# Performance work log

Hardware: AMD Instinct MI355X
Metric: run time of the kernel (lower is better)

The kernel has to match this reference:

```python
import jax, jax.numpy as jnp
import numpy as np

B, T, E, H, S = 64, 128, 256, 512, 1024


def setup_inputs() -> dict:
    key = jax.random.key(0)
    ks = jax.random.split(key, 14)
    p = lambda k, shape, s=0.05: jax.random.normal(k, shape, dtype=jnp.float32) * s
    return {
        "embedded_inputs": jax.random.normal(ks[0], (B, T, E), dtype=jnp.float32),
        "h0": jax.random.normal(ks[1], (B, H), dtype=jnp.float32),
        "c0": jax.random.normal(ks[2], (B, H), dtype=jnp.float32),
        "context": jax.random.normal(ks[3], (B, S, H), dtype=jnp.float32),
        "W_ih": p(ks[4], (E, 4 * H)),
        "b_ih": p(ks[5], (4 * H,)),
        "W_hh": p(ks[6], (H, 4 * H)),
        "b_hh": p(ks[7], (4 * H,)),
        "W_out": p(ks[8], (2 * H, H)),
        "b_out": p(ks[9], (H,)),
        "W_ax": p(ks[10], (H + E, H)),
        "b_ax": p(ks[11], (H,)),
        "W_pg": p(ks[12], (4 * H, 1)),
        "b_pg": p(ks[13], (1,)),
    }


def reference(embedded_inputs, h0, c0, context, W_ih, b_ih, W_hh, b_hh,
              W_out, b_out, W_ax, b_ax, W_pg, b_pg):
    # mask positions where the encoder output is all-zero padding
    ctx_mask = jnp.mean(context, axis=-1) == 0  # [B,S]

    def step(carry, x):  # x: [B,E]
        h, c = carry
        gates = x @ W_ih + b_ih + h @ W_hh + b_hh          # [B,4H]
        i, f, g, o = jnp.split(gates, 4, axis=-1)
        c_t = jax.nn.sigmoid(f) * c + jax.nn.sigmoid(i) * jnp.tanh(g)
        h_t = jax.nn.sigmoid(o) * jnp.tanh(c_t)            # [B,H]
        # dot attention
        scores = jnp.einsum('bsh,bh->bs', context, h_t)    # [B,S]
        scores = jnp.where(ctx_mask, -jnp.inf, scores)
        attn_dist = jax.nn.softmax(scores, axis=1)         # [B,S]
        attn_ctx = jnp.einsum('bsh,bs->bh', context, attn_dist)  # [B,H]
        xa = jnp.concatenate([attn_ctx, x], axis=-1) @ W_ax + b_ax   # [B,H]
        out = jnp.concatenate([attn_ctx, h_t], axis=-1) @ W_out + b_out  # [B,H]
        p_gen = jax.nn.sigmoid(
            jnp.concatenate([attn_ctx, h_t, c_t, xa], axis=-1) @ W_pg + b_pg)  # [B,1]
        return (h_t, c_t), (out, attn_dist, p_gen)

    xs = jnp.swapaxes(embedded_inputs, 0, 1)  # [T,B,E]
    (h, c), (outputs, attn_dists, p_gens) = jax.lax.scan(step, (h0, c0), xs)
    return outputs, h, c, attn_dists, p_gens
```

## Files before the change

kernel.cpp:

```cpp
#include <hip/hip_runtime.h>

#define T_ 128
#define B_ 64
#define E_ 256
#define H_ 512
#define S_ 1024
#define G_ 2048
#define NCH 6
#define NBLK 512
#define ABLK 128
#define BLK 256
#define NGRP 16
#define BH (B_*H_)
#define PSTR 520
#define PARTBUF (B_*NCH*PSTR)

#define U_ARR   256
#define U_TOTAL (U_ARR + NBLK*16)

#define F_V1   8704
#define F_VX   (F_V1 + 512)
#define F_S0   (F_VX + 256)
#define F_H3   (F_S0 + 64)
#define F_C3   (F_H3 + 3*BH)
#define F_SC2  (F_C3 + 3*BH)
#define F_PART (F_SC2 + 2*B_*S_)
#define F_CTX16 (F_PART + 2*PARTBUF)
#define WS_MIN_BYTES ((size_t)F_CTX16*4)
#define WS_BF16_BYTES ((size_t)F_CTX16*4 + (size_t)B_*S_*H_*2)

#define O_OUT 0
#define O_H   ((size_t)T_*B_*H_)
#define O_C   (O_H + BH)
#define O_AD  (O_C + BH)
#define O_PG  (O_AD + (size_t)T_*B_*S_)

#define S_ACT   0
#define S_PART  3088
#define S_GATE  4112
#define SB_RED  0
#define SB_ML   2080
#define SB_BIAS 2088
#define C_ACTX  5136
#define C_H2    5648
#define C_PRT   6160
#define C_TMP   6416
#define C_V1    6424
#define POOLSZ  7200

#define NEG_INF (-__builtin_inff())

__device__ __forceinline__ float sigm(float x){ return 1.f/(1.f+__expf(-x)); }
__device__ __forceinline__ float tanh_(float x){ return 1.f - 2.f/(1.f+__expf(2.f*x)); }
__device__ __forceinline__ float wred(float v){
#pragma unroll
  for (int m = 1; m < 64; m <<= 1) v += __shfl_xor(v, m, 64);
  return v;
}
__device__ __forceinline__ float ald(const float* p){
  return __hip_atomic_load(p, __ATOMIC_RELAXED, __HIP_MEMORY_SCOPE_AGENT);
}
__device__ __forceinline__ void ast(float* p, float v){
  __hip_atomic_store(p, v, __ATOMIC_RELAXED, __HIP_MEMORY_SCOPE_AGENT);
}
__device__ __forceinline__ void ast64(unsigned long long* p, unsigned long long v){
  __hip_atomic_store(p, v, __ATOMIC_RELAXED, __HIP_MEMORY_SCOPE_AGENT);
}
__device__ __forceinline__ unsigned short b16rne(float f){
  unsigned u = __float_as_uint(f);
  unsigned r = u + 0x7fffu + ((u >> 16) & 1u);
  return (unsigned short)(r >> 16);
}
__device__ __forceinline__ void unp(unsigned w, float& lo, float& hi){
  lo = __uint_as_float(w << 16);
  hi = __uint_as_float(w & 0xffff0000u);
}

__device__ __forceinline__ void gbar(unsigned* W, unsigned ep){
  __syncthreads();
  const int tid = threadIdx.x, bid = blockIdx.x;
  if (tid == 0) {
    asm volatile("s_waitcnt vmcnt(0)" ::: "memory");
    __hip_atomic_store(&W[U_ARR + bid*16], ep, __ATOMIC_RELAXED, __HIP_MEMORY_SCOPE_AGENT);
  }
  if (bid == 0) {
    const int i0 = tid*2, i1 = i0+1;
    while (__hip_atomic_load(&W[U_ARR + i0*16], __ATOMIC_RELAXED, __HIP_MEMORY_SCOPE_AGENT) < ep)
      __builtin_amdgcn_s_sleep(2);
    while (__hip_atomic_load(&W[U_ARR + i1*16], __ATOMIC_RELAXED, __HIP_MEMORY_SCOPE_AGENT) < ep)
      __builtin_amdgcn_s_sleep(2);
    __syncthreads();
    if (tid < NGRP)
      __hip_atomic_store(&W[tid*16], ep, __ATOMIC_RELAXED, __HIP_MEMORY_SCOPE_AGENT);
  }
  if (tid == 0) {
    while (__hip_atomic_load(&W[(bid>>5)*16], __ATOMIC_RELAXED, __HIP_MEMORY_SCOPE_AGENT) < ep)
      __builtin_amdgcn_s_sleep(4);
  }
  __syncthreads();
}

__device__ void do_A(int t, int bid, int tid,
                     const float* __restrict__ emb, const float* __restrict__ Wih,
                     const float* __restrict__ bih, const float* __restrict__ Whh,
                     const float* __restrict__ bhh, float* __restrict__ F,
                     float* __restrict__ pool)
{
  const int bg = bid >> 3, ug = bid & 7;
  {
    const int r = tid >> 6, i = tid & 63;
    const float* xr = emb + ((size_t)(bg*4 + r)*T_ + t)*E_ + i*4;
    *(float4*)(pool + S_ACT + r*772 + i*4) = *(const float4*)xr;
    const float* hsrc = F + F_H3 + ((t+2)%3)*BH + (size_t)(bg*4 + r)*H_ + i*8;
    float4 h0v, h1v;
    h0v.x=ald(hsrc+0); h0v.y=ald(hsrc+1); h0v.z=ald(hsrc+2); h0v.w=ald(hsrc+3);
    h1v.x=ald(hsrc+4); h1v.y=ald(hsrc+5); h1v.z=ald(hsrc+6); h1v.w=ald(hsrc+7);
    *(float4*)(pool + S_ACT + r*772 + 256 + i*8)     = h0v;
    *(float4*)(pool + S_ACT + r*772 + 256 + i*8 + 4) = h1v;
  }
  __syncthreads();
  const int ks = tid >> 7, bl = (tid >> 5) & 3, cq = tid & 31;
  const int cgi1 = cq, cgi2 = cq + 32;
  const int col1 = ((cgi1 >> 4) << 9) + ug*64 + ((cgi1 & 15) << 2);
  const int col2 = ((cgi2 >> 4) << 9) + ug*64 + ((cgi2 & 15) << 2);
  float4 A1, A2;
  if (ks == 0) {
    const float4 x1 = *(const float4*)(bih + col1), y1 = *(const float4*)(bhh + col1);
    const float4 x2 = *(const float4*)(bih + col2), y2 = *(const float4*)(bhh + col2);
    A1.x=x1.x+y1.x; A1.y=x1.y+y1.y; A1.z=x1.z+y1.z; A1.w=x1.w+y1.w;
    A2.x=x2.x+y2.x; A2.y=x2.y+y2.y; A2.z=x2.z+y2.z; A2.w=x2.w+y2.w;
  } else { A1.x=A1.y=A1.z=A1.w=0.f; A2.x=A2.y=A2.z=A2.w=0.f; }
  const float* ap = pool + S_ACT + bl*772;
  if (ks == 0) {
    const float* w1 = Wih + col1; const float* w2 = Wih + col2;
#pragma unroll 8
    for (int k = 0; k < 256; ++k) {
      float a = ap[k];
      float4 v1 = *(const float4*)(w1 + (size_t)k*G_);
      float4 v2 = *(const float4*)(w2 + (size_t)k*G_);
      A1.x=fmaf(a,v1.x,A1.x); A1.y=fmaf(a,v1.y,A1.y); A1.z=fmaf(a,v1.z,A1.z); A1.w=fmaf(a,v1.w,A1.w);
      A2.x=fmaf(a,v2.x,A2.x); A2.y=fmaf(a,v2.y,A2.y); A2.z=fmaf(a,v2.z,A2.z); A2.w=fmaf(a,v2.w,A2.w);
    }
    const float* u1 = Whh + col1; const float* u2 = Whh + col2;
    const float* ap2 = ap + 256;
#pragma unroll 8
    for (int k = 0; k < 128; ++k) {
      float a = ap2[k];
      float4 v1 = *(const float4*)(u1 + (size_t)k*G_);
      float4 v2 = *(const float4*)(u2 + (size_t)k*G_);
      A1.x=fmaf(a,v1.x,A1.x); A1.y=fmaf(a,v1.y,A1.y); A1.z=fmaf(a,v1.z,A1.z); A1.w=fmaf(a,v1.w,A1.w);
      A2.x=fmaf(a,v2.x,A2.x); A2.y=fmaf(a,v2.y,A2.y); A2.z=fmaf(a,v2.z,A2.z); A2.w=fmaf(a,v2.w,A2.w);
    }
  } else {
    const float* u1 = Whh + (size_t)128*G_ + col1; const float* u2 = Whh + (size_t)128*G_ + col2;
    const float* ap2 = ap + 384;
#pragma unroll 8
    for (int k = 0; k < 384; ++k) {
      float a = ap2[k];
      float4 v1 = *(const float4*)(u1 + (size_t)k*G_);
      float4 v2 = *(const float4*)(u2 + (size_t)k*G_);
      A1.x=fmaf(a,v1.x,A1.x); A1.y=fmaf(a,v1.y,A1.y); A1.z=fmaf(a,v1.z,A1.z); A1.w=fmaf(a,v1.w,A1.w);
      A2.x=fmaf(a,v2.x,A2.x); A2.y=fmaf(a,v2.y,A2.y); A2.z=fmaf(a,v2.z,A2.z); A2.w=fmaf(a,v2.w,A2.w);
    }
  }
  if (ks == 1) {
    *(float4*)(pool + S_PART + ((bl*64 + cgi1) << 2)) = A1;
    *(float4*)(pool + S_PART + ((bl*64 + cgi2) << 2)) = A2;
  }
  __syncthreads();
  if (ks == 0) {
    const float4 P1 = *(const float4*)(pool + S_PART + ((bl*64 + cgi1) << 2));
    const float4 P2 = *(const float4*)(pool + S_PART + ((bl*64 + cgi2) << 2));
    A1.x+=P1.x; A1.y+=P1.y; A1.z+=P1.z; A1.w+=P1.w;
    A2.x+=P2.x; A2.y+=P2.y; A2.z+=P2.z; A2.w+=P2.w;
    *(float4*)(pool + S_GATE + bl*256 + (cgi1 << 2)) = A1;
    *(float4*)(pool + S_GATE + bl*256 + (cgi2 << 2)) = A2;
  }
  __syncthreads();
  {
    const int bl2 = tid >> 6, ul = tid & 63;
    const int b2 = bg*4 + bl2, uu = ug*64 + ul;
    float gi = pool[S_GATE + bl2*256 + ul];
    float gf = pool[S_GATE + bl2*256 + 64 + ul];
    float gg = pool[S_GATE + bl2*256 + 128 + ul];
    float go = pool[S_GATE + bl2*256 + 192 + ul];
    float cp = ald(F + F_C3 + ((t+2)%3)*BH + (size_t)b2*H_ + uu);
    float cn = sigm(gf)*cp + sigm(gi)*tanh_(gg);
    float hn = sigm(go)*tanh_(cn);
    ast(F + F_H3 + (t%3)*BH + (size_t)b2*H_ + uu, hn);
    ast(F + F_C3 + (t%3)*BH + (size_t)b2*H_ + uu, cn);
  }
}

template<bool BF16>
__device__ void do_B(int t, int bid, int tid, const float* __restrict__ ctx,
                     float* __restrict__ F, float* __restrict__ pool)
{
  const int idx = bid - ABLK;
  const int b = idx / NCH, ch = idx - b*NCH;
  const int sb = (ch*S_)/NCH, se = ((ch+1)*S_)/NCH;
  const int w = tid >> 6, lane = tid & 63;
  const float* hb = F + F_H3 + (t%3)*BH + (size_t)b*H_ + lane*8;
  float h0_=ald(hb+0), h1_=ald(hb+1), h2_=ald(hb+2), h3_=ald(hb+3),
        h4_=ald(hb+4), h5_=ald(hb+5), h6_=ald(hb+6), h7_=ald(hb+7);
  float* scw = F + F_SC2 + (size_t)(t&1)*(B_*S_) + (size_t)b*S_;
  const float* s_bias = pool + SB_BIAS;

  if (BF16) {
    const uint4* c16v = (const uint4*)(F + F_CTX16) + (size_t)b*S_*64 + lane;
    float l = 0.f;
    float a0=0,a1=0,a2=0,a3=0,a4=0,a5=0,a6=0,a7=0;
    for (int s0 = sb + w*16; s0 < se; s0 += 64) {
      uint4 q[16];
#pragma unroll
      for (int i = 0; i < 16; ++i) {
        int s = s0 + i;
        int ss = (s < se) ? s : sb;
        q[i] = c16v[(size_t)ss*64];
      }
#pragma unroll
      for (int hh = 0; hh < 2; ++hh) {
        const int o = hh*8;
        float d[8];
#pragma unroll
        for (int i = 0; i < 8; ++i) {
          float c0,c1,c2,c3,c4,c5,c6,c7;
          unp(q[o+i].x,c0,c1); unp(q[o+i].y,c2,c3); unp(q[o+i].z,c4,c5); unp(q[o+i].w,c6,c7);
          d[i] = c0*h0_+c1*h1_+c2*h2_+c3*h3_+c4*h4_+c5*h5_+c6*h6_+c7*h7_;
        }
#pragma unroll
        for (int mm = 1; mm < 64; mm <<= 1) {
          d[0]+=__shfl_xor(d[0],mm,64); d[1]+=__shfl_xor(d[1],mm,64);
          d[2]+=__shfl_xor(d[2],mm,64); d[3]+=__shfl_xor(d[3],mm,64);
          d[4]+=__shfl_xor(d[4],mm,64); d[5]+=__shfl_xor(d[5],mm,64);
          d[6]+=__shfl_xor(d[6],mm,64); d[7]+=__shfl_xor(d[7],mm,64);
        }
        float wg[8];
#pragma unroll
        for (int i = 0; i < 8; ++i) {
          int s = s0 + o + i;
          bool v = (s < se);
          float bias = v ? s_bias[s - sb] : NEG_INF;
          float sc = d[i] + bias;
          if (lane == 0 && v) ast(scw + s, sc);
          wg[i] = (bias == 0.f) ? __expf(fminf(sc, 80.f)) : 0.f;
          l += wg[i];
        }
#pragma unroll
        for (int i = 0; i < 8; ++i) {
          float c0,c1,c2,c3,c4,c5,c6,c7;
          unp(q[o+i].x,c0,c1); unp(q[o+i].y,c2,c3); unp(q[o+i].z,c4,c5); unp(q[o+i].w,c6,c7);
          a0=fmaf(wg[i],c0,a0); a1=fmaf(wg[i],c1,a1); a2=fmaf(wg[i],c2,a2); a3=fmaf(wg[i],c3,a3);
          a4=fmaf(wg[i],c4,a4); a5=fmaf(wg[i],c5,a5); a6=fmaf(wg[i],c6,a6); a7=fmaf(wg[i],c7,a7);
        }
      }
    }
    if (lane == 0) pool[SB_ML + w] = l;
    { float* r = pool + SB_RED + w*520 + lane*8;
      r[0]=a0; r[1]=a1; r[2]=a2; r[3]=a3; r[4]=a4; r[5]=a5; r[6]=a6; r[7]=a7; }
    __syncthreads();
    float lb = pool[SB_ML+0]+pool[SB_ML+1]+pool[SB_ML+2]+pool[SB_ML+3];
    float* Pp = F + F_PART + (size_t)(t&1)*PARTBUF + (size_t)(b*NCH+ch)*PSTR;
    for (int u = tid; u < H_; u += BLK)
      ast(Pp + 8 + u, pool[SB_RED + 0*520 + u] + pool[SB_RED + 1*520 + u]
                    + pool[SB_RED + 2*520 + u] + pool[SB_RED + 3*520 + u]);
    if (tid == 0) { ast(Pp+0, 0.f); ast(Pp+1, lb); }
    return;
  }

  const float* cbase = ctx + (size_t)b*S_*H_ + lane*8;
  float m = NEG_INF, l = 0.f;
  float a0=0,a1=0,a2=0,a3=0,a4=0,a5=0,a6=0,a7=0;
  for (int s0 = sb + w*4; s0 < se; s0 += 16) {
    float cv[4][8]; float d[4];
#pragma unroll
    for (int i = 0; i < 4; ++i) {
      int s = s0 + i;
      const float* cr = cbase + (size_t)(s < se ? s : sb)*H_;
      float4 cA = *(const float4*)cr, cB = *(const float4*)(cr + 4);
      cv[i][0]=cA.x; cv[i][1]=cA.y; cv[i][2]=cA.z; cv[i][3]=cA.w;
      cv[i][4]=cB.x; cv[i][5]=cB.y; cv[i][6]=cB.z; cv[i][7]=cB.w;
    }
#pragma unroll
    for (int i = 0; i < 4; ++i)
      d[i] = cv[i][0]*h0_ + cv[i][1]*h1_ + cv[i][2]*h2_ + cv[i][3]*h3_
           + cv[i][4]*h4_ + cv[i][5]*h5_ + cv[i][6]*h6_ + cv[i][7]*h7_;
#pragma unroll
    for (int mm = 1; mm < 64; mm <<= 1) {
      d[0] += __shfl_xor(d[0], mm, 64); d[1] += __shfl_xor(d[1], mm, 64);
      d[2] += __shfl_xor(d[2], mm, 64); d[3] += __shfl_xor(d[3], mm, 64);
    }
    float sc[4];
#pragma unroll
    for (int i = 0; i < 4; ++i) {
      int s = s0 + i;
      sc[i] = (s < se) ? d[i] + s_bias[s - sb] : NEG_INF;
      if (lane == 0 && s < se) ast(scw + s, sc[i]);
    }
    float mx = fmaxf(fmaxf(sc[0],sc[1]), fmaxf(sc[2],sc[3]));
    float mn = fmaxf(m, mx);
    float al = (mn == m) ? 1.f : __expf(m - mn);
    float w0 = (sc[0]==NEG_INF)?0.f:__expf(sc[0]-mn);
    float w1 = (sc[1]==NEG_INF)?0.f:__expf(sc[1]-mn);
    float w2 = (sc[2]==NEG_INF)?0.f:__expf(sc[2]-mn);
    float w3 = (sc[3]==NEG_INF)?0.f:__expf(sc[3]-mn);
    l = l*al + (w0+w1+w2+w3);
    a0 = a0*al + w0*cv[0][0] + w1*cv[1][0] + w2*cv[2][0] + w3*cv[3][0];
    a1 = a1*al + w0*cv[0][1] + w1*cv[1][1] + w2*cv[2][1] + w3*cv[3][1];
    a2 = a2*al + w0*cv[0][2] + w1*cv[1][2] + w2*cv[2][2] + w3*cv[3][2];
    a3 = a3*al + w0*cv[0][3] + w1*cv[1][3] + w2*cv[2][3] + w3*cv[3][3];
    a4 = a4*al + w0*cv[0][4] + w1*cv[1][4] + w2*cv[2][4] + w3*cv[3][4];
    a5 = a5*al + w0*cv[0][5] + w1*cv[1][5] + w2*cv[2][5] + w3*cv[3][5];
    a6 = a6*al + w0*cv[0][6] + w1*cv[1][6] + w2*cv[2][6] + w3*cv[3][6];
    a7 = a7*al + w0*cv[0][7] + w1*cv[1][7] + w2*cv[2][7] + w3*cv[3][7];
    m = mn;
  }
  if (lane == 0) { pool[SB_ML + w*2] = m; pool[SB_ML + w*2+1] = l; }
  { float* r = pool + SB_RED + w*520 + lane*8;
    r[0]=a0; r[1]=a1; r[2]=a2; r[3]=a3; r[4]=a4; r[5]=a5; r[6]=a6; r[7]=a7; }
  __syncthreads();
  float m0=pool[SB_ML+0], l0=pool[SB_ML+1], m1=pool[SB_ML+2], l1=pool[SB_ML+3],
        m2=pool[SB_ML+4], l2=pool[SB_ML+5], m3=pool[SB_ML+6], l3=pool[SB_ML+7];
  float mb = fmaxf(fmaxf(m0,m1), fmaxf(m2,m3));
  float k0 = (l0>0.f) ? __expf(m0-mb) : 0.f;
  float k1 = (l1>0.f) ? __expf(m1-mb) : 0.f;
  float k2 = (l2>0.f) ? __expf(m2-mb) : 0.f;
  float k3 = (l3>0.f) ? __expf(m3-mb) : 0.f;
  float lb = k0*l0 + k1*l1 + k2*l2 + k3*l3;
  float* Pp = F + F_PART + (size_t)(t&1)*PARTBUF + (size_t)(b*NCH+ch)*PSTR;
  for (int u = tid; u < H_; u += BLK)
    ast(Pp + 8 + u, k0*pool[SB_RED + 0*520 + u] + k1*pool[SB_RED + 1*520 + u]
                  + k2*pool[SB_RED + 2*520 + u] + k3*pool[SB_RED + 3*520 + u]);
  if (tid == 0) { ast(Pp+0, mb); ast(Pp+1, lb); }
}

__device__ void do_C(int tc, int bid, int tid,
                     const float* __restrict__ emb, const float* __restrict__ Wout,
                     const float* __restrict__ bout, const float* __restrict__ Wpg,
                     float* __restrict__ out, float* __restrict__ F,
                     float* __restrict__ pool)
{
  const int b = bid >> 1, p = bid & 1;
  const float* P0 = F + F_PART + (size_t)(tc&1)*PARTBUF + (size_t)(b*NCH)*PSTR;
  float mk[NCH], lk[NCH], ck[NCH];
  float mb = NEG_INF;
#pragma unroll
  for (int k = 0; k < NCH; ++k) { mk[k]=ald(P0+k*PSTR); lk[k]=ald(P0+k*PSTR+1); mb=fmaxf(mb,mk[k]); }
  float lb = 0.f;
#pragma unroll
  for (int k = 0; k < NCH; ++k) { ck[k] = (lk[k]>0.f) ? __expf(mk[k]-mb) : 0.f; lb += ck[k]*lk[k]; }
  float inv = 1.f/lb;
  {
    int u = tid;
    float v0 = 0.f, v1 = 0.f;
#pragma unroll
    for (int k = 0; k < NCH; ++k) {
      v0 += ck[k]*ald(P0 + k*PSTR + 8 + u);
      v1 += ck[k]*ald(P0 + k*PSTR + 8 + u + 256);
    }
    pool[C_ACTX + u]       = v0*inv;
    pool[C_ACTX + u + 256] = v1*inv;
    const float* hsrc = F + F_H3 + (tc%3)*BH + (size_t)b*H_;
    pool[C_H2 + tid]       = ald(hsrc + tid);
    pool[C_H2 + tid + 256] = ald(hsrc + tid + 256);
  }
  __syncthreads();
  {
    const float* scr = F + F_SC2 + (size_t)(tc&1)*(B_*S_) + (size_t)b*S_;
    float* ad = out + O_AD + ((size_t)tc*B_ + b)*S_;
    int s = p*512 + tid;
    ad[s] = __expf(ald(scr+s)-mb)*inv;
    s += 256;
    ad[s] = __expf(ald(scr+s)-mb)*inv;
  }
  {
    const int kh = tid >> 7, jj = tid & 127;
    const int j = p*256 + jj;
    float acc0 = (kh == 0) ? bout[j]     : 0.f;
    float acc1 = (kh == 0) ? bout[j+128] : 0.f;
    const float* src = (kh == 0) ? (pool + C_ACTX) : (pool + C_H2);
    const float* wq = Wout + (size_t)(kh*512)*H_ + j;
#pragma unroll 8
    for (int k = 0; k < 512; ++k) {
      float s = src[k];
      const float* r = wq + (size_t)k*H_;
      acc0 = fmaf(s, r[0],   acc0);
      acc1 = fmaf(s, r[128], acc1);
    }
    if (kh == 1) { pool[C_PRT + jj*2] = acc0; pool[C_PRT + jj*2 + 1] = acc1; }
    __syncthreads();
    if (kh == 0) {
      acc0 += pool[C_PRT + jj*2];
      acc1 += pool[C_PRT + jj*2 + 1];
      out[O_OUT + ((size_t)tc*B_ + b)*H_ + j]       = acc0;
      out[O_OUT + ((size_t)tc*B_ + b)*H_ + j + 128] = acc1;
    }
  }
  if (p == 0) {
    const float* cb = F + F_C3 + (tc%3)*BH + (size_t)b*H_;
    const float* xr = emb + ((size_t)b*T_ + tc)*E_;
    float part = 0.f;
#pragma unroll
    for (int jj2 = 0; jj2 < 7; ++jj2) {
      int i = tid + jj2*BLK;
      float v;
      if (i < 512)       v = pool[C_ACTX + i]     * pool[C_V1 + i];
      else if (i < 1024) v = pool[C_H2 + i - 512] * Wpg[i];
      else if (i < 1536) v = ald(cb + i - 1024)   * Wpg[i];
      else               v = xr[i - 1536]         * pool[C_V1 + 512 + (i - 1536)];
      part += v;
    }
    part = wred(part);
    if ((tid & 63) == 0) pool[C_TMP + (tid>>6)] = part;
    __syncthreads();
    if (tid == 0)
      out[O_PG + (size_t)tc*B_ + b] =
        sigm(pool[C_TMP]+pool[C_TMP+1]+pool[C_TMP+2]+pool[C_TMP+3] + pool[C_V1 + 768]);
  }
}

template<bool BF16>
__global__ __launch_bounds__(BLK, 2)
void decoder_kernel(const float* __restrict__ emb, const float* __restrict__ h0,
                    const float* __restrict__ c0, const float* __restrict__ ctx,
                    const float* __restrict__ Wih, const float* __restrict__ bih,
                    const float* __restrict__ Whh, const float* __restrict__ bhh,
                    const float* __restrict__ Wout, const float* __restrict__ bout,
                    const float* __restrict__ Wax, const float* __restrict__ bax,
                    const float* __restrict__ Wpg, const float* __restrict__ bpg,
                    float* __restrict__ out, float* __restrict__ F)
{
  __shared__ float pool[POOLSZ];
  unsigned* W = (unsigned*)F;
  const int tid = threadIdx.x, bid = blockIdx.x;
  unsigned ep = 0;

  if (bid < 128) {
    int i = bid*BLK + tid;
    ast(F + F_H3 + 2*BH + i, h0[i]);
    ast(F + F_C3 + 2*BH + i, c0[i]);
  }
  if (bid >= ABLK) {
    const int idx = bid - ABLK;
    const int b = idx / NCH, ch = idx - b*NCH;
    const int sb = (ch*S_)/NCH, se = ((ch+1)*S_)/NCH;
    const int w = tid >> 6, lane = tid & 63;
    for (int s = sb + w; s < se; s += 4) {
      const float* cr = ctx + ((size_t)b*S_ + s)*H_ + lane*8;
      float4 cA = *(const float4*)cr, cB = *(const float4*)(cr+4);
      float ssum = cA.x+cA.y+cA.z+cA.w+cB.x+cB.y+cB.z+cB.w;
      ssum = wred(ssum);
      if (lane == 0) pool[SB_BIAS + (s-sb)] = (ssum == 0.f) ? NEG_INF : 0.f;
    }
  }
  if (BF16) {
    unsigned long long* dst = (unsigned long long*)(F + F_CTX16);
    size_t base = (size_t)bid*BLK + tid;
#pragma unroll 2
    for (int it = 0; it < 32; ++it) {
      size_t ci = base + (size_t)it*131072;
      const float4 v0 = *(const float4*)(ctx + ci*8);
      const float4 v1 = *(const float4*)(ctx + ci*8 + 4);
      unsigned long long lo = (unsigned long long)b16rne(v0.x)
        | ((unsigned long long)b16rne(v0.y) << 16)
        | ((unsigned long long)b16rne(v0.z) << 32)
        | ((unsigned long long)b16rne(v0.w) << 48);
      unsigned long long hi = (unsigned long long)b16rne(v1.x)
        | ((unsigned long long)b16rne(v1.y) << 16)
        | ((unsigned long long)b16rne(v1.z) << 32)
        | ((unsigned long long)b16rne(v1.w) << 48);
      ast64(dst + ci*2, lo);
      ast64(dst + ci*2 + 1, hi);
    }
  }
  if (bid < 5) {
    const int w = tid>>6, lane = tid&63;
    const float* wp = Wpg + 1536 + lane*8;
    float4 wA = *(const float4*)wp, wB = *(const float4*)(wp+4);
    if (bid < 4) {
      for (int rr = 0; rr < 32; ++rr) {
        int k = bid*128 + rr*4 + w;
        const float* ar = Wax + (size_t)k*H_ + lane*8;
        float4 xA = *(const float4*)ar, xB = *(const float4*)(ar+4);
        float d = xA.x*wA.x+xA.y*wA.y+xA.z*wA.z+xA.w*wA.w
                + xB.x*wB.x+xB.y*wB.y+xB.z*wB.z+xB.w*wB.w;
        d = wred(d);
        if (lane == 0) ast(F + F_V1 + k, Wpg[k] + d);
      }
    } else {
      for (int rr = 0; rr < 64; ++rr) {
        int k = rr*4 + w;
        const float* ar = Wax + (size_t)(512+k)*H_ + lane*8;
        float4 xA = *(const float4*)ar, xB = *(const float4*)(ar+4);
        float d = xA.x*wA.x+xA.y*wA.y+xA.z*wA.z+xA.w*wA.w
                + xB.x*wB.x+xB.y*wB.y+xB.z*wB.z+xB.w*wB.w;
        d = wred(d);
        if (lane == 0) ast(F + F_VX + k, d);
      }
      if (tid < 64) {
        const float* br = bax + lane*8;
        float4 bA = *(const float4*)br, bB = *(const float4*)(br+4);
        float d = bA.x*wA.x+bA.y*wA.y+bA.z*wA.z+bA.w*wA.w
                + bB.x*wB.x+bB.y*wB.y+bB.z*wB.z+bB.w*wB.w;
        d = wred(d);
        if (lane == 0) ast(F + F_S0, bpg[0] + d);
      }
    }
  }
  gbar(W, ++ep);

  if (bid < ABLK) {
    for (int i = tid; i < 769; i += BLK)
      pool[C_V1 + i] = ald(F + F_V1 + i);
  }

  if (bid < ABLK) do_A(0, bid, tid, emb, Wih, bih, Whh, bhh, F, pool);
  gbar(W, ++ep);

  for (int t = 0; t < T_; ++t) {
    if (bid >= ABLK) {
      do_B<BF16>(t, bid, tid, ctx, F, pool);
    } else {
      if (t < T_-1) do_A(t+1, bid, tid, emb, Wih, bih, Whh, bhh, F, pool);
      if (t > 0)    do_C(t-1, bid, tid, emb, Wout, bout, Wpg, out, F, pool);
    }
    gbar(W, ++ep);
  }

  if (bid < ABLK) {
    do_C(T_-1, bid, tid, emb, Wout, bout, Wpg, out, F, pool);
  } else {
    const int idx = bid - ABLK;
    if (idx < 128) {
      int i = idx*BLK + tid;
      out[O_H + i] = ald(F + F_H3 + 1*BH + i);
    } else if (idx < 256) {
      int i = (idx-128)*BLK + tid;
      out[O_C + i] = ald(F + F_C3 + 1*BH + i);
    }
  }
}

extern "C" void kernel_launch(void* const* d_in, const int* in_sizes, int n_in,
                              void* d_out, int out_size, void* d_ws, size_t ws_size,
                              hipStream_t stream)
{
  if (ws_size < WS_MIN_BYTES) return;
  hipMemsetAsync(d_ws, 0, U_TOTAL * sizeof(unsigned), stream);
  if (ws_size >= WS_BF16_BYTES) {
    decoder_kernel<true><<<dim3(NBLK), dim3(BLK), 0, stream>>>(
        (const float*)d_in[0],  (const float*)d_in[1],  (const float*)d_in[2],
        (const float*)d_in[3],  (const float*)d_in[4],  (const float*)d_in[5],
        (const float*)d_in[6],  (const float*)d_in[7],  (const float*)d_in[8],
        (const float*)d_in[9],  (const float*)d_in[10], (const float*)d_in[11],
        (const float*)d_in[12], (const float*)d_in[13],
        (float*)d_out, (float*)d_ws);
  } else {
    decoder_kernel<false><<<dim3(NBLK), dim3(BLK), 0, stream>>>(
        (const float*)d_in[0],  (const float*)d_in[1],  (const float*)d_in[2],
        (const float*)d_in[3],  (const float*)d_in[4],  (const float*)d_in[5],
        (const float*)d_in[6],  (const float*)d_in[7],  (const float*)d_in[8],
        (const float*)d_in[9],  (const float*)d_in[10], (const float*)d_in[11],
        (const float*)d_in[12], (const float*)d_in[13],
        (float*)d_out, (float*)d_ws);
  }
}
```

Measured before the change: 8.117 ms.

## Keep each attention block's bf16 context slice resident in registers across timesteps

The attention blocks now load their bf16 context rows (44 rows of uint4 per lane) into registers once before the time loop, and reuse them for every one of the 128 steps instead of re-reading context from global memory each step. The A/C and B block loops are split into separate per-role loops that each call the grid barrier, and a trailing __syncthreads is added to the B routines. The cost is much higher register pressure (176 VGPRs for the context alone), which risks spilling or lower occupancy. The rest of the kernel structure is unchanged.

```diff
diff --git a/kernel.cpp b/kernel.cpp
--- a/kernel.cpp
+++ b/kernel.cpp
@@ -74,6 +74,11 @@
 __device__ __forceinline__ void unp(unsigned w, float& lo, float& hi){
   lo = __uint_as_float(w << 16);
   hi = __uint_as_float(w & 0xffff0000u);
+}
+__device__ __forceinline__ unsigned long long pk8(const float4& v0, const float4& v1, int sel){
+  const float4& v = sel ? v1 : v0;
+  return (unsigned long long)b16rne(v.x) | ((unsigned long long)b16rne(v.y) << 16)
+       | ((unsigned long long)b16rne(v.z) << 32) | ((unsigned long long)b16rne(v.w) << 48);
 }
 
 __device__ __forceinline__ void gbar(unsigned* W, unsigned ep){
@@ -192,9 +197,77 @@
   }
 }
 
-template<bool BF16>
-__device__ void do_B(int t, int bid, int tid, const float* __restrict__ ctx,
-                     float* __restrict__ F, float* __restrict__ pool)
+__device__ __forceinline__ void do_B_reg(int t, int tid, int b, int sb, int se,
+                                         int base_row, int w, int lane,
+                                         uint4 (&creg)[44],
+                                         float* __restrict__ F,
+                                         float* __restrict__ pool, int ch)
+{
+  const float* hb = F + F_H3 + (t%3)*BH + (size_t)b*H_ + lane*8;
+  float h0_=ald(hb+0), h1_=ald(hb+1), h2_=ald(hb+2), h3_=ald(hb+3),
+        h4_=ald(hb+4), h5_=ald(hb+5), h6_=ald(hb+6), h7_=ald(hb+7);
+  float* scw = F + F_SC2 + (size_t)(t&1)*(B_*S_) + (size_t)b*S_;
+  const float* s_bias = pool + SB_BIAS;
+  float l = 0.f;
+  float a0=0,a1=0,a2=0,a3=0,a4=0,a5=0,a6=0,a7=0;
+#pragma unroll
+  for (int g = 0; g < 6; ++g) {
+    const int RG = (g < 5) ? 8 : 4;
+    float d[8], wg[8];
+#pragma unroll
+    for (int j = 0; j < 8; ++j) {
+      if (j >= RG) continue;
+      float c0,c1,c2,c3,c4,c5,c6,c7;
+      unp(creg[g*8+j].x,c0,c1); unp(creg[g*8+j].y,c2,c3);
+      unp(creg[g*8+j].z,c4,c5); unp(creg[g*8+j].w,c6,c7);
+      d[j] = c0*h0_+c1*h1_+c2*h2_+c3*h3_+c4*h4_+c5*h5_+c6*h6_+c7*h7_;
+    }
+#pragma unroll
+    for (int mm = 1; mm < 64; mm <<= 1) {
+      d[0]+=__shfl_xor(d[0],mm,64); d[1]+=__shfl_xor(d[1],mm,64);
+      d[2]+=__shfl_xor(d[2],mm,64); d[3]+=__shfl_xor(d[3],mm,64);
+      if (RG == 8) {
+        d[4]+=__shfl_xor(d[4],mm,64); d[5]+=__shfl_xor(d[5],mm,64);
+        d[6]+=__shfl_xor(d[6],mm,64); d[7]+=__shfl_xor(d[7],mm,64);
+      }
+    }
+#pragma unroll
+    for (int j = 0; j < 8; ++j) {
+      if (j >= RG) continue;
+      const int i = g*8 + j;
+      const int s = base_row + i;
+      const bool v = (i < 43) && (s < se);
+      float bias = v ? s_bias[s - sb] : NEG_INF;
+      float sc = d[j] + bias;
+      if (lane == 0 && v) ast(scw + s, sc);
+      wg[j] = (bias == 0.f) ? __expf(fminf(sc, 80.f)) : 0.f;
+      l += wg[j];
+    }
+#pragma unroll
+    for (int j = 0; j < 8; ++j) {
+      if (j >= RG) continue;
+      float c0,c1,c2,c3,c4,c5,c6,c7;
+      unp(creg[g*8+j].x,c0,c1); unp(creg[g*8+j].y,c2,c3);
+      unp(creg[g*8+j].z,c4,c5); unp(creg[g*8+j].w,c6,c7);
+      a0=fmaf(wg[j],c0,a0); a1=fmaf(wg[j],c1,a1); a2=fmaf(wg[j],c2,a2); a3=fmaf(wg[j],c3,a3);
+      a4=fmaf(wg[j],c4,a4); a5=fmaf(wg[j],c5,a5); a6=fmaf(wg[j],c6,a6); a7=fmaf(wg[j],c7,a7);
+    }
+  }
+  if (lane == 0) pool[SB_ML + w] = l;
+  { float* r = pool + SB_RED + w*520 + lane*8;
+    r[0]=a0; r[1]=a1; r[2]=a2; r[3]=a3; r[4]=a4; r[5]=a5; r[6]=a6; r[7]=a7; }
+  __syncthreads();
+  float lb = pool[SB_ML+0]+pool[SB_ML+1]+pool[SB_ML+2]+pool[SB_ML+3];
+  float* Pp = F + F_PART + (size_t)(t&1)*PARTBUF + (size_t)(b*NCH+ch)*PSTR;
+  for (int u = tid; u < H_; u += BLK)
+    ast(Pp + 8 + u, pool[SB_RED + 0*520 + u] + pool[SB_RED + 1*520 + u]
+                  + pool[SB_RED + 2*520 + u] + pool[SB_RED + 3*520 + u]);
+  if (tid == 0) { ast(Pp+0, 0.f); ast(Pp+1, lb); }
+  __syncthreads();
+}
+
+__device__ void do_B_f32(int t, int bid, int tid, const float* __restrict__ ctx,
+                         float* __restrict__ F, float* __restrict__ pool)
 {
   const int idx = bid - ABLK;
   const int b = idx / NCH, ch = idx - b*NCH;
@@ -205,69 +278,6 @@
         h4_=ald(hb+4), h5_=ald(hb+5), h6_=ald(hb+6), h7_=ald(hb+7);
   float* scw = F + F_SC2 + (size_t)(t&1)*(B_*S_) + (size_t)b*S_;
   const float* s_bias = pool + SB_BIAS;
-
-  if (BF16) {
-    const uint4* c16v = (const uint4*)(F + F_CTX16) + (size_t)b*S_*64 + lane;
-    float l = 0.f;
-    float a0=0,a1=0,a2=0,a3=0,a4=0,a5=0,a6=0,a7=0;
-    for (int s0 = sb + w*16; s0 < se; s0 += 64) {
-      uint4 q[16];
-#pragma unroll
-      for (int i = 0; i < 16; ++i) {
-        int s = s0 + i;
-        int ss = (s < se) ? s : sb;
-        q[i] = c16v[(size_t)ss*64];
-      }
-#pragma unroll
-      for (int hh = 0; hh < 2; ++hh) {
-        const int o = hh*8;
-        float d[8];
-#pragma unroll
-        for (int i = 0; i < 8; ++i) {
-          float c0,c1,c2,c3,c4,c5,c6,c7;
-          unp(q[o+i].x,c0,c1); unp(q[o+i].y,c2,c3); unp(q[o+i].z,c4,c5); unp(q[o+i].w,c6,c7);
-          d[i] = c0*h0_+c1*h1_+c2*h2_+c3*h3_+c4*h4_+c5*h5_+c6*h6_+c7*h7_;
-        }
-#pragma unroll
-        for (int mm = 1; mm < 64; mm <<= 1) {
-          d[0]+=__shfl_xor(d[0],mm,64); d[1]+=__shfl_xor(d[1],mm,64);
-          d[2]+=__shfl_xor(d[2],mm,64); d[3]+=__shfl_xor(d[3],mm,64);
-          d[4]+=__shfl_xor(d[4],mm,64); d[5]+=__shfl_xor(d[5],mm,64);
-          d[6]+=__shfl_xor(d[6],mm,64); d[7]+=__shfl_xor(d[7],mm,64);
-        }
-        float wg[8];
-#pragma unroll
-        for (int i = 0; i < 8; ++i) {
-          int s = s0 + o + i;
-          bool v = (s < se);
-          float bias = v ? s_bias[s - sb] : NEG_INF;
-          float sc = d[i] + bias;
-          if (lane == 0 && v) ast(scw + s, sc);
-          wg[i] = (bias == 0.f) ? __expf(fminf(sc, 80.f)) : 0.f;
-          l += wg[i];
-        }
-#pragma unroll
-        for (int i = 0; i < 8; ++i) {
-          float c0,c1,c2,c3,c4,c5,c6,c7;
-          unp(q[o+i].x,c0,c1); unp(q[o+i].y,c2,c3); unp(q[o+i].z,c4,c5); unp(q[o+i].w,c6,c7);
-          a0=fmaf(wg[i],c0,a0); a1=fmaf(wg[i],c1,a1); a2=fmaf(wg[i],c2,a2); a3=fmaf(wg[i],c3,a3);
-          a4=fmaf(wg[i],c4,a4); a5=fmaf(wg[i],c5,a5); a6=fmaf(wg[i],c6,a6); a7=fmaf(wg[i],c7,a7);
-        }
-      }
-    }
-    if (lane == 0) pool[SB_ML + w] = l;
-    { float* r = pool + SB_RED + w*520 + lane*8;
-      r[0]=a0; r[1]=a1; r[2]=a2; r[3]=a3; r[4]=a4; r[5]=a5; r[6]=a6; r[7]=a7; }
-    __syncthreads();
-    float lb = pool[SB_ML+0]+pool[SB_ML+1]+pool[SB_ML+2]+pool[SB_ML+3];
-    float* Pp = F + F_PART + (size_t)(t&1)*PARTBUF + (size_t)(b*NCH+ch)*PSTR;
-    for (int u = tid; u < H_; u += BLK)
-      ast(Pp + 8 + u, pool[SB_RED + 0*520 + u] + pool[SB_RED + 1*520 + u]
-                    + pool[SB_RED + 2*520 + u] + pool[SB_RED + 3*520 + u]);
-    if (tid == 0) { ast(Pp+0, 0.f); ast(Pp+1, lb); }
-    return;
-  }
-
   const float* cbase = ctx + (size_t)b*S_*H_ + lane*8;
   float m = NEG_INF, l = 0.f;
   float a0=0,a1=0,a2=0,a3=0,a4=0,a5=0,a6=0,a7=0;
@@ -332,6 +342,7 @@
     ast(Pp + 8 + u, k0*pool[SB_RED + 0*520 + u] + k1*pool[SB_RED + 1*520 + u]
                   + k2*pool[SB_RED + 2*520 + u] + k3*pool[SB_RED + 3*520 + u]);
   if (tid == 0) { ast(Pp+0, mb); ast(Pp+1, lb); }
+  __syncthreads();
 }
 
 __device__ void do_C(int tc, int bid, int tid,
@@ -461,16 +472,8 @@
       size_t ci = base + (size_t)it*131072;
       const float4 v0 = *(const float4*)(ctx + ci*8);
       const float4 v1 = *(const float4*)(ctx + ci*8 + 4);
-      unsigned long long lo = (unsigned long long)b16rne(v0.x)
-        | ((unsigned long long)b16rne(v0.y) << 16)
-        | ((unsigned long long)b16rne(v0.z) << 32)
-        | ((unsigned long long)b16rne(v0.w) << 48);
-      unsigned long long hi = (unsigned long long)b16rne(v1.x)
-        | ((unsigned long long)b16rne(v1.y) << 16)
-        | ((unsigned long long)b16rne(v1.z) << 32)
-        | ((unsigned long long)b16rne(v1.w) << 48);
-      ast64(dst + ci*2, lo);
-      ast64(dst + ci*2 + 1, hi);
+      ast64(dst + ci*2,     pk8(v0, v1, 0));
+      ast64(dst + ci*2 + 1, pk8(v0, v1, 1));
     }
   }
   if (bid < 5) {
@@ -512,24 +515,45 @@
   if (bid < ABLK) {
     for (int i = tid; i < 769; i += BLK)
       pool[C_V1 + i] = ald(F + F_V1 + i);
-  }
-
-  if (bid < ABLK) do_A(0, bid, tid, emb, Wih, bih, Whh, bhh, F, pool);
-  gbar(W, ++ep);
-
-  for (int t = 0; t < T_; ++t) {
-    if (bid >= ABLK) {
-      do_B<BF16>(t, bid, tid, ctx, F, pool);
-    } else {
+    do_A(0, bid, tid, emb, Wih, bih, Whh, bhh, F, pool);
+    gbar(W, ++ep);
+    for (int t = 0; t < T_; ++t) {
       if (t < T_-1) do_A(t+1, bid, tid, emb, Wih, bih, Whh, bhh, F, pool);
       if (t > 0)    do_C(t-1, bid, tid, emb, Wout, bout, Wpg, out, F, pool);
+      gbar(W, ++ep);
+    }
+    do_C(T_-1, bid, tid, emb, Wout, bout, Wpg, out, F, pool);
+  } else if (BF16) {
+    const int idx = bid - ABLK;
+    const int b = idx / NCH, ch = idx - b*NCH;
+    const int sb = (ch*S_)/NCH, se = ((ch+1)*S_)/NCH;
+    const int w = tid >> 6, lane = tid & 63;
+    const int base_row = sb + 43*w;
+    const uint4* c16v = (const uint4*)(F + F_CTX16) + (size_t)b*S_*64 + lane;
+    uint4 creg[44];
+#pragma unroll
+    for (int i = 0; i < 44; ++i) {
+      int r = base_row + i;
+      creg[i] = c16v[(size_t)((r < se) ? r : sb)*64];
     }
     gbar(W, ++ep);
-  }
-
-  if (bid < ABLK) {
-    do_C(T_-1, bid, tid, emb, Wout, bout, Wpg, out, F, pool);
+    for (int t = 0; t < T_; ++t) {
+      do_B_reg(t, tid, b, sb, se, base_row, w, lane, creg, F, pool, ch);
+      gbar(W, ++ep);
+    }
+    if (idx < 128) {
+      int i = idx*BLK + tid;
+      out[O_H + i] = ald(F + F_H3 + 1*BH + i);
+    } else if (idx < 256) {
+      int i = (idx-128)*BLK + tid;
+      out[O_C + i] = ald(F + F_C3 + 1*BH + i);
+    }
   } else {
+    gbar(W, ++ep);
+    for (int t = 0; t < T_; ++t) {
+      do_B_f32(t, bid, tid, ctx, F, pool);
+      gbar(W, ++ep);
+    }
     const int idx = bid - ABLK;
     if (idx < 128) {
       int i = idx*BLK + tid;
@@ -547,21 +571,17 @@
 {
   if (ws_size < WS_MIN_BYTES) return;
   hipMemsetAsync(d_ws, 0, U_TOTAL * sizeof(unsigned), stream);
+#define ARGS \
+      (const float*)d_in[0],  (const float*)d_in[1],  (const float*)d_in[2],   \
+      (const float*)d_in[3],  (const float*)d_in[4],  (const float*)d_in[5],   \
+      (const float*)d_in[6],  (const float*)d_in[7],  (const float*)d_in[8],   \
+      (const float*)d_in[9],  (const float*)d_in[10], (const float*)d_in[11],  \
+      (const float*)d_in[12], (const float*)d_in[13],                          \
+      (float*)d_out, (float*)d_ws
   if (ws_size >= WS_BF16_BYTES) {
-    decoder_kernel<true><<<dim3(NBLK), dim3(BLK), 0, stream>>>(
-        (const float*)d_in[0],  (const float*)d_in[1],  (const float*)d_in[2],
-        (const float*)d_in[3],  (const float*)d_in[4],  (const float*)d_in[5],
-        (const float*)d_in[6],  (const float*)d_in[7],  (const float*)d_in[8],
-        (const float*)d_in[9],  (const float*)d_in[10], (const float*)d_in[11],
-        (const float*)d_in[12], (const float*)d_in[13],
-        (float*)d_out, (float*)d_ws);
+    decoder_kernel<true><<<dim3(NBLK), dim3(BLK), 0, stream>>>(ARGS);
   } else {
-    decoder_kernel<false><<<dim3(NBLK), dim3(BLK), 0, stream>>>(
-        (const float*)d_in[0],  (const float*)d_in[1],  (const float*)d_in[2],
-        (const float*)d_in[3],  (const float*)d_in[4],  (const float*)d_in[5],
-        (const float*)d_in[6],  (const float*)d_in[7],  (const float*)d_in[8],
-        (const float*)d_in[9],  (const float*)d_in[10], (const float*)d_in[11],
-        (const float*)d_in[12], (const float*)d_in[13],
-        (float*)d_out, (float*)d_ws);
-  }
-}
+    decoder_kernel<false><<<dim3(NBLK), dim3(BLK), 0, stream>>>(ARGS);
+  }
+#undef ARGS
+}
```

After: 17.35 ms. 2.14x slower.
